# Performance work log

Measured on AMD Instinct MI355X. Metric: run time of the kernel, lower is better.

## Reference

```python
import jax, jax.numpy as jnp
import numpy as np

NUM_HEADS = 8

def setup_inputs() -> dict:
    key = jax.random.key(0)
    qkv = jax.random.normal(key, (8, 1536, 2048), dtype=jnp.float32)
    return {"qkv": qkv}

def reference(qkv) -> jnp.ndarray:
    bs, width, length = qkv.shape
    ch = width // (3 * NUM_HEADS)
    qkv_r = qkv.reshape(bs * NUM_HEADS, 3 * ch, length)
    q, k, v = jnp.split(qkv_r, 3, axis=1)  # each [bs*H, ch, length]
    scale = 1.0 / jnp.sqrt(jnp.sqrt(jnp.float32(ch)))
    # scores [bs*H, t, s]
    weight = jnp.einsum('bct,bcs->bts', q * scale, k * scale)
    weight = jax.nn.softmax(weight.astype(jnp.float32), axis=-1).astype(qkv.dtype)
    a = jnp.einsum('bts,bcs->bct', weight, v)  # [bs*H, ch, length]
    return a.reshape(bs, -1, length)
```

## Files before the change

### kernel.cpp

```cpp
#include <hip/hip_runtime.h>
#include <hip/hip_fp16.h>


typedef _Float16 half8 __attribute__((ext_vector_type(8)));
typedef _Float16 half4 __attribute__((ext_vector_type(4)));
typedef float floatx4 __attribute__((ext_vector_type(4)));

__global__ __launch_bounds__(256, 4) void attn_kernel(const float* __restrict__ qkv,
                                                      float* __restrict__ out)
{
    __shared__ _Float16 Kt[64 * 64];
    __shared__ _Float16 Vt[64 * 64];
    __shared__ _Float16 Pt[128 * 64];

    const int tid  = threadIdx.x;
    const int wave = tid >> 6;
    const int lane = tid & 63;
    const int llo  = lane & 15;
    const int lhi  = lane >> 4;

    const int blk  = blockIdx.x;
    const int slot = blk >> 3;
    const int bh   = (blk & 7) * 8 + (slot >> 4);
    const int tile = slot & 15;
    const int t0   = tile * 128;

    const float* qb = qkv + (size_t)bh * 393216;
    const float* kb = qb + 131072;
    const float* vb = qb + 262144;

    const float C  = 0.125f * 1.44269504088896f;
    const float B2 = 6.0f;

    half8 qf[2][2];
    const int twbase = t0 + wave * 32;
    #pragma unroll
    for (int nt = 0; nt < 2; ++nt) {
        const int t = twbase + nt * 16 + llo;
        #pragma unroll
        for (int ck = 0; ck < 2; ++ck)
            #pragma unroll
            for (int j = 0; j < 8; ++j) {
                const int c = ck * 32 + lhi * 8 + j;
                qf[nt][ck][j] = (_Float16)(qb[c * 2048 + t] * C);
            }
    }

    const int kc4 = (tid >> 4) * 4;
    const int ksq = (tid & 15) * 4;
    const int vc  = tid >> 4;
    const int vs  = (tid & 15) * 4;

    int kwoff[4];
    #pragma unroll
    for (int sr = 0; sr < 4; ++sr) {
        const int s  = ksq + sr;
        const int sw = ((s >> 2) ^ s) & 7;
        kwoff[sr] = s * 64 + ((((kc4 >> 3) ^ sw) & 7) << 3) + (kc4 & 7);
    }
    int vwoff[4];
    #pragma unroll
    for (int i = 0; i < 4; ++i) {
        const int c = vc + 16 * i;
        vwoff[i] = c * 64 + ((((vs >> 3) ^ (c & 7)) & 7) << 3) + (vs & 7);
    }
    int kroff[4][2];
    #pragma unroll
    for (int ms = 0; ms < 4; ++ms) {
        const int s  = ms * 16 + llo;
        const int sw = ((s >> 2) ^ s) & 7;
        kroff[ms][0] = s * 64 + (((lhi ^ sw) & 7) << 3);
        kroff[ms][1] = s * 64 + ((((lhi + 4) ^ sw) & 7) << 3);
    }
    int pwoff[2][4];
    #pragma unroll
    for (int nt = 0; nt < 2; ++nt) {
        const int row = wave * 32 + nt * 16 + llo;
        #pragma unroll
        for (int ms = 0; ms < 4; ++ms)
            pwoff[nt][ms] = row * 64 + ((((2 * ms + (lhi >> 1)) ^ (llo & 7)) & 7) << 3)
                          + 4 * (lhi & 1);
    }
    int proff[2][2];
    #pragma unroll
    for (int nt = 0; nt < 2; ++nt) {
        const int row = wave * 32 + nt * 16 + llo;
        #pragma unroll
        for (int sk = 0; sk < 2; ++sk)
            proff[nt][sk] = row * 64 + ((((sk * 4 + lhi) ^ (llo & 7)) & 7) << 3);
    }
    int vroff[4][2];
    #pragma unroll
    for (int mc = 0; mc < 4; ++mc) {
        const int row = mc * 16 + llo;
        #pragma unroll
        for (int sk = 0; sk < 2; ++sk)
            vroff[mc][sk] = row * 64 + ((((sk * 4 + lhi) ^ (llo & 7)) & 7) << 3);
    }

    floatx4 kr[4], vr[4];
    auto loadKV = [&](int s0) {
        #pragma unroll
        for (int r = 0; r < 4; ++r)
            kr[r] = *reinterpret_cast<const floatx4*>(kb + (kc4 + r) * 2048 + s0 + ksq);
        #pragma unroll
        for (int i = 0; i < 4; ++i)
            vr[i] = *reinterpret_cast<const floatx4*>(vb + (vc + 16 * i) * 2048 + s0 + vs);
    };
    auto storeKV = [&]() {
        #pragma unroll
        for (int sr = 0; sr < 4; ++sr) {
            half4 h = { (_Float16)kr[0][sr], (_Float16)kr[1][sr],
                        (_Float16)kr[2][sr], (_Float16)kr[3][sr] };
            *reinterpret_cast<half4*>(&Kt[kwoff[sr]]) = h;
        }
        #pragma unroll
        for (int i = 0; i < 4; ++i) {
            half4 h = { (_Float16)vr[i][0], (_Float16)vr[i][1],
                        (_Float16)vr[i][2], (_Float16)vr[i][3] };
            *reinterpret_cast<half4*>(&Vt[vwoff[i]]) = h;
        }
    };

    floatx4 O[2][4];
    #pragma unroll
    for (int nt = 0; nt < 2; ++nt)
        #pragma unroll
        for (int mc = 0; mc < 4; ++mc)
            O[nt][mc] = (floatx4){0.f, 0.f, 0.f, 0.f};
    float l_run[2] = {0.f, 0.f};

    loadKV(0);

    for (int it = 0; it < 32; ++it) {
        __syncthreads();
        storeKV();
        __syncthreads();
        if (it + 1 < 32) loadKV((it + 1) * 64);

        #pragma unroll
        for (int ms = 0; ms < 4; ++ms) {
            half8 a0 = *reinterpret_cast<const half8*>(&Kt[kroff[ms][0]]);
            half8 a1 = *reinterpret_cast<const half8*>(&Kt[kroff[ms][1]]);
            #pragma unroll
            for (int nt = 0; nt < 2; ++nt) {
                floatx4 acc = (floatx4){-B2, -B2, -B2, -B2};
                acc = __builtin_amdgcn_mfma_f32_16x16x32_f16(a0, qf[nt][0], acc, 0, 0, 0);
                acc = __builtin_amdgcn_mfma_f32_16x16x32_f16(a1, qf[nt][1], acc, 0, 0, 0);
                half4 ph;
                float l = 0.f;
                #pragma unroll
                for (int r = 0; r < 4; ++r) {
                    const float p = __builtin_amdgcn_exp2f(acc[r]);
                    l += p;
                    ph[r] = (_Float16)p;
                }
                l_run[nt] += l;
                *reinterpret_cast<half4*>(&Pt[pwoff[nt][ms]]) = ph;
            }
        }

        #pragma unroll
        for (int sk = 0; sk < 2; ++sk) {
            half8 bp[2];
            #pragma unroll
            for (int nt = 0; nt < 2; ++nt)
                bp[nt] = *reinterpret_cast<const half8*>(&Pt[proff[nt][sk]]);
            #pragma unroll
            for (int mc = 0; mc < 4; ++mc) {
                half8 av = *reinterpret_cast<const half8*>(&Vt[vroff[mc][sk]]);
                #pragma unroll
                for (int nt = 0; nt < 2; ++nt)
                    O[nt][mc] = __builtin_amdgcn_mfma_f32_16x16x32_f16(av, bp[nt], O[nt][mc], 0, 0, 0);
            }
        }
    }

    float* ob = out + (size_t)bh * 131072;
    #pragma unroll
    for (int nt = 0; nt < 2; ++nt) {
        float l = l_run[nt];
        l += __shfl_xor(l, 16, 64);
        l += __shfl_xor(l, 32, 64);
        const float inv = 1.0f / l;
        const int t = twbase + nt * 16 + llo;
        #pragma unroll
        for (int mc = 0; mc < 4; ++mc)
            #pragma unroll
            for (int r = 0; r < 4; ++r) {
                const int c = mc * 16 + lhi * 4 + r;
                ob[c * 2048 + t] = O[nt][mc][r] * inv;
            }
    }
}

extern "C" void kernel_launch(void* const* d_in, const int* in_sizes, int n_in,
                              void* d_out, int out_size, void* d_ws, size_t ws_size,
                              hipStream_t stream) {
    const float* qkv = (const float*)d_in[0];
    float* out = (float*)d_out;
    attn_kernel<<<dim3(1024), dim3(256), 0, stream>>>(qkv, out);
}
```

Before: 221.2 us.

## Keep softmax probabilities in registers and feed 16x16x16 MFMA directly

Removes the shared-memory round trip for the probability tile P. The exp outputs of the QK^T MFMA are packed to fp16 in registers and used directly as the B operand of 16x16x16 MFMAs for the PV product, with the V reads laid out to match. It also switches the fp32-to-fp16 conversions to packed round-toward-zero conversions. This drops LDS traffic and the Pt buffer, which lowers shared memory use. In exchange it issues twice as many smaller-K MFMAs and uses RTZ rounding instead of round-to-nearest.

```diff
diff --git a/kernel.cpp b/kernel.cpp
--- a/kernel.cpp
+++ b/kernel.cpp
@@ -4,6 +4,7 @@
 
 typedef _Float16 half8 __attribute__((ext_vector_type(8)));
 typedef _Float16 half4 __attribute__((ext_vector_type(4)));
+typedef _Float16 half2_t __attribute__((ext_vector_type(2)));
 typedef float floatx4 __attribute__((ext_vector_type(4)));
 
 __global__ __launch_bounds__(256, 4) void attn_kernel(const float* __restrict__ qkv,
@@ -11,7 +12,6 @@
 {
     __shared__ _Float16 Kt[64 * 64];
     __shared__ _Float16 Vt[64 * 64];
-    __shared__ _Float16 Pt[128 * 64];
 
     const int tid  = threadIdx.x;
     const int wave = tid >> 6;
@@ -72,30 +72,11 @@
         kroff[ms][0] = s * 64 + (((lhi ^ sw) & 7) << 3);
         kroff[ms][1] = s * 64 + ((((lhi + 4) ^ sw) & 7) << 3);
     }
-    int pwoff[2][4];
+    int vroff_in[4];
     #pragma unroll
-    for (int nt = 0; nt < 2; ++nt) {
-        const int row = wave * 32 + nt * 16 + llo;
-        #pragma unroll
-        for (int ms = 0; ms < 4; ++ms)
-            pwoff[nt][ms] = row * 64 + ((((2 * ms + (lhi >> 1)) ^ (llo & 7)) & 7) << 3)
-                          + 4 * (lhi & 1);
-    }
-    int proff[2][2];
-    #pragma unroll
-    for (int nt = 0; nt < 2; ++nt) {
-        const int row = wave * 32 + nt * 16 + llo;
-        #pragma unroll
-        for (int sk = 0; sk < 2; ++sk)
-            proff[nt][sk] = row * 64 + ((((sk * 4 + lhi) ^ (llo & 7)) & 7) << 3);
-    }
-    int vroff[4][2];
-    #pragma unroll
-    for (int mc = 0; mc < 4; ++mc) {
-        const int row = mc * 16 + llo;
-        #pragma unroll
-        for (int sk = 0; sk < 2; ++sk)
-            vroff[mc][sk] = row * 64 + ((((sk * 4 + lhi) ^ (llo & 7)) & 7) << 3);
+    for (int ms = 0; ms < 4; ++ms) {
+        const int pg = ((2 * ms + (lhi >> 1)) ^ (llo & 7)) & 7;
+        vroff_in[ms] = llo * 64 + (pg << 3) + ((lhi & 1) << 2);
     }
 
     floatx4 kr[4], vr[4];
@@ -110,14 +91,16 @@
     auto storeKV = [&]() {
         #pragma unroll
         for (int sr = 0; sr < 4; ++sr) {
-            half4 h = { (_Float16)kr[0][sr], (_Float16)kr[1][sr],
-                        (_Float16)kr[2][sr], (_Float16)kr[3][sr] };
+            half2_t lo = __builtin_bit_cast(half2_t, __builtin_amdgcn_cvt_pkrtz(kr[0][sr], kr[1][sr]));
+            half2_t hi = __builtin_bit_cast(half2_t, __builtin_amdgcn_cvt_pkrtz(kr[2][sr], kr[3][sr]));
+            half4 h = { lo[0], lo[1], hi[0], hi[1] };
             *reinterpret_cast<half4*>(&Kt[kwoff[sr]]) = h;
         }
         #pragma unroll
         for (int i = 0; i < 4; ++i) {
-            half4 h = { (_Float16)vr[i][0], (_Float16)vr[i][1],
-                        (_Float16)vr[i][2], (_Float16)vr[i][3] };
+            half2_t lo = __builtin_bit_cast(half2_t, __builtin_amdgcn_cvt_pkrtz(vr[i][0], vr[i][1]));
+            half2_t hi = __builtin_bit_cast(half2_t, __builtin_amdgcn_cvt_pkrtz(vr[i][2], vr[i][3]));
+            half4 h = { lo[0], lo[1], hi[0], hi[1] };
             *reinterpret_cast<half4*>(&Vt[vwoff[i]]) = h;
         }
     };
@@ -142,36 +125,26 @@
         for (int ms = 0; ms < 4; ++ms) {
             half8 a0 = *reinterpret_cast<const half8*>(&Kt[kroff[ms][0]]);
             half8 a1 = *reinterpret_cast<const half8*>(&Kt[kroff[ms][1]]);
+            half4 pf[2];
             #pragma unroll
             for (int nt = 0; nt < 2; ++nt) {
                 floatx4 acc = (floatx4){-B2, -B2, -B2, -B2};
                 acc = __builtin_amdgcn_mfma_f32_16x16x32_f16(a0, qf[nt][0], acc, 0, 0, 0);
                 acc = __builtin_amdgcn_mfma_f32_16x16x32_f16(a1, qf[nt][1], acc, 0, 0, 0);
-                half4 ph;
-                float l = 0.f;
-                #pragma unroll
-                for (int r = 0; r < 4; ++r) {
-                    const float p = __builtin_amdgcn_exp2f(acc[r]);
-                    l += p;
-                    ph[r] = (_Float16)p;
-                }
-                l_run[nt] += l;
-                *reinterpret_cast<half4*>(&Pt[pwoff[nt][ms]]) = ph;
+                const float p0 = __builtin_amdgcn_exp2f(acc[0]);
+                const float p1 = __builtin_amdgcn_exp2f(acc[1]);
+                const float p2 = __builtin_amdgcn_exp2f(acc[2]);
+                const float p3 = __builtin_amdgcn_exp2f(acc[3]);
+                l_run[nt] += (p0 + p1) + (p2 + p3);
+                half2_t lo = __builtin_bit_cast(half2_t, __builtin_amdgcn_cvt_pkrtz(p0, p1));
+                half2_t hi = __builtin_bit_cast(half2_t, __builtin_amdgcn_cvt_pkrtz(p2, p3));
+                pf[nt] = (half4){ lo[0], lo[1], hi[0], hi[1] };
             }
-        }
-
-        #pragma unroll
-        for (int sk = 0; sk < 2; ++sk) {
-            half8 bp[2];
-            #pragma unroll
-            for (int nt = 0; nt < 2; ++nt)
-                bp[nt] = *reinterpret_cast<const half8*>(&Pt[proff[nt][sk]]);
             #pragma unroll
             for (int mc = 0; mc < 4; ++mc) {
-                half8 av = *reinterpret_cast<const half8*>(&Vt[vroff[mc][sk]]);
-                #pragma unroll
-                for (int nt = 0; nt < 2; ++nt)
-                    O[nt][mc] = __builtin_amdgcn_mfma_f32_16x16x32_f16(av, bp[nt], O[nt][mc], 0, 0, 0);
+                half4 av = *reinterpret_cast<const half4*>(&Vt[mc * 1024 + vroff_in[ms]]);
+                O[0][mc] = __builtin_amdgcn_mfma_f32_16x16x16f16(av, pf[0], O[0][mc], 0, 0, 0);
+                O[1][mc] = __builtin_amdgcn_mfma_f32_16x16x16f16(av, pf[1], O[1][mc], 0, 0, 0);
             }
         }
     }
```

Result: slower. 239.0 us (+8.1%).

## Pre-convert K/V to swizzled fp16 and stream tiles via global_load_lds double buffer

Applied to the files above, without the earlier changes.

Adds a prep kernel that converts K and V to fp16 once, in the swizzled LDS tile layout, and stores them in the workspace. The attention kernel then DMAs those tiles directly into double-buffered LDS with global_load_lds, which drops the per-block fp32 loads, conversions and LDS stores along with one barrier per iteration. Softmax conversion now uses packed cvt_pkrtz. This costs an extra launch plus workspace traffic, and doubles the LDS used for K/V, which may reduce occupancy.

```diff
diff --git a/kernel.cpp b/kernel.cpp
--- a/kernel.cpp
+++ b/kernel.cpp
@@ -4,14 +4,68 @@
 
 typedef _Float16 half8 __attribute__((ext_vector_type(8)));
 typedef _Float16 half4 __attribute__((ext_vector_type(4)));
+typedef _Float16 half2_t __attribute__((ext_vector_type(2)));
 typedef float floatx4 __attribute__((ext_vector_type(4)));
 
+#define AS1 __attribute__((address_space(1)))
+#define AS3 __attribute__((address_space(3)))
+#define GLLDS(g, l) __builtin_amdgcn_global_load_lds((const AS1 void*)(g), (AS3 void*)(l), 16, 0, 0)
+
+__global__ __launch_bounds__(256) void prep_kernel(const float* __restrict__ qkv,
+                                                   _Float16* __restrict__ ws16)
+{
+    const int tid   = threadIdx.x;
+    const int blk   = blockIdx.x;
+    const int bh    = blk >> 5;
+    const int stile = blk & 31;
+    const int s0    = stile * 64;
+
+    const float* kb = qkv + (size_t)bh * 393216 + 131072;
+    const float* vb = qkv + (size_t)bh * 393216 + 262144;
+    _Float16* wk = ws16 + (size_t)bh * 262144 + stile * 4096;
+    _Float16* wv = wk + 131072;
+
+    const int kc4 = (tid >> 4) * 4;
+    const int ksq = (tid & 15) * 4;
+    const int vc  = tid >> 4;
+    const int vs  = (tid & 15) * 4;
+
+    floatx4 kr[4], vr[4];
+    #pragma unroll
+    for (int r = 0; r < 4; ++r)
+        kr[r] = *reinterpret_cast<const floatx4*>(kb + (kc4 + r) * 2048 + s0 + ksq);
+    #pragma unroll
+    for (int i = 0; i < 4; ++i)
+        vr[i] = *reinterpret_cast<const floatx4*>(vb + (vc + 16 * i) * 2048 + s0 + vs);
+
+    #pragma unroll
+    for (int sr = 0; sr < 4; ++sr) {
+        const int s  = ksq + sr;
+        const int sw = ((s >> 2) ^ s) & 7;
+        const int off = s * 64 + ((((kc4 >> 3) ^ sw) & 7) << 3) + (kc4 & 7);
+        half2_t lo = __builtin_bit_cast(half2_t, __builtin_amdgcn_cvt_pkrtz(kr[0][sr], kr[1][sr]));
+        half2_t hi = __builtin_bit_cast(half2_t, __builtin_amdgcn_cvt_pkrtz(kr[2][sr], kr[3][sr]));
+        half4 h = { lo[0], lo[1], hi[0], hi[1] };
+        *reinterpret_cast<half4*>(&wk[off]) = h;
+    }
+    #pragma unroll
+    for (int i = 0; i < 4; ++i) {
+        const int c = vc + 16 * i;
+        const int off = c * 64 + ((((vs >> 3) ^ (c & 7)) & 7) << 3) + (vs & 7);
+        half2_t lo = __builtin_bit_cast(half2_t, __builtin_amdgcn_cvt_pkrtz(vr[i][0], vr[i][1]));
+        half2_t hi = __builtin_bit_cast(half2_t, __builtin_amdgcn_cvt_pkrtz(vr[i][2], vr[i][3]));
+        half4 h = { lo[0], lo[1], hi[0], hi[1] };
+        *reinterpret_cast<half4*>(&wv[off]) = h;
+    }
+}
+
 __global__ __launch_bounds__(256, 4) void attn_kernel(const float* __restrict__ qkv,
+                                                      const _Float16* __restrict__ ws16,
                                                       float* __restrict__ out)
 {
-    __shared__ _Float16 Kt[64 * 64];
-    __shared__ _Float16 Vt[64 * 64];
-    __shared__ _Float16 Pt[128 * 64];
+    __shared__ _Float16 KtB[2][4096];
+    __shared__ _Float16 VtB[2][4096];
+    __shared__ _Float16 Pt[8192];
 
     const int tid  = threadIdx.x;
     const int wave = tid >> 6;
@@ -26,8 +80,8 @@
     const int t0   = tile * 128;
 
     const float* qb = qkv + (size_t)bh * 393216;
-    const float* kb = qb + 131072;
-    const float* vb = qb + 262144;
+    const _Float16* wkt = ws16 + (size_t)bh * 262144;
+    const _Float16* wvt = wkt + 131072;
 
     const float C  = 0.125f * 1.44269504088896f;
     const float B2 = 6.0f;
@@ -46,24 +100,6 @@
             }
     }
 
-    const int kc4 = (tid >> 4) * 4;
-    const int ksq = (tid & 15) * 4;
-    const int vc  = tid >> 4;
-    const int vs  = (tid & 15) * 4;
-
-    int kwoff[4];
-    #pragma unroll
-    for (int sr = 0; sr < 4; ++sr) {
-        const int s  = ksq + sr;
-        const int sw = ((s >> 2) ^ s) & 7;
-        kwoff[sr] = s * 64 + ((((kc4 >> 3) ^ sw) & 7) << 3) + (kc4 & 7);
-    }
-    int vwoff[4];
-    #pragma unroll
-    for (int i = 0; i < 4; ++i) {
-        const int c = vc + 16 * i;
-        vwoff[i] = c * 64 + ((((vs >> 3) ^ (c & 7)) & 7) << 3) + (vs & 7);
-    }
     int kroff[4][2];
     #pragma unroll
     for (int ms = 0; ms < 4; ++ms) {
@@ -98,28 +134,15 @@
             vroff[mc][sk] = row * 64 + ((((sk * 4 + lhi) ^ (llo & 7)) & 7) << 3);
     }
 
-    floatx4 kr[4], vr[4];
-    auto loadKV = [&](int s0) {
-        #pragma unroll
-        for (int r = 0; r < 4; ++r)
-            kr[r] = *reinterpret_cast<const floatx4*>(kb + (kc4 + r) * 2048 + s0 + ksq);
-        #pragma unroll
-        for (int i = 0; i < 4; ++i)
-            vr[i] = *reinterpret_cast<const floatx4*>(vb + (vc + 16 * i) * 2048 + s0 + vs);
-    };
-    auto storeKV = [&]() {
-        #pragma unroll
-        for (int sr = 0; sr < 4; ++sr) {
-            half4 h = { (_Float16)kr[0][sr], (_Float16)kr[1][sr],
-                        (_Float16)kr[2][sr], (_Float16)kr[3][sr] };
-            *reinterpret_cast<half4*>(&Kt[kwoff[sr]]) = h;
-        }
-        #pragma unroll
-        for (int i = 0; i < 4; ++i) {
-            half4 h = { (_Float16)vr[i][0], (_Float16)vr[i][1],
-                        (_Float16)vr[i][2], (_Float16)vr[i][3] };
-            *reinterpret_cast<half4*>(&Vt[vwoff[i]]) = h;
-        }
+    auto dma = [&](int it, int b) {
+        const char* gk = (const char*)(wkt + it * 4096) + wave * 2048 + lane * 16;
+        const char* gv = (const char*)(wvt + it * 4096) + wave * 2048 + lane * 16;
+        char* lk = (char*)(&KtB[b][0]) + wave * 2048;
+        char* lv = (char*)(&VtB[b][0]) + wave * 2048;
+        GLLDS(gk,        lk);
+        GLLDS(gk + 1024, lk + 1024);
+        GLLDS(gv,        lv);
+        GLLDS(gv + 1024, lv + 1024);
     };
 
     floatx4 O[2][4];
@@ -130,13 +153,14 @@
             O[nt][mc] = (floatx4){0.f, 0.f, 0.f, 0.f};
     float l_run[2] = {0.f, 0.f};
 
-    loadKV(0);
+    dma(0, 0);
+    __syncthreads();
 
     for (int it = 0; it < 32; ++it) {
-        __syncthreads();
-        storeKV();
-        __syncthreads();
-        if (it + 1 < 32) loadKV((it + 1) * 64);
+        if (it + 1 < 32) dma(it + 1, (it + 1) & 1);
+
+        const _Float16* Kt = KtB[it & 1];
+        const _Float16* Vt = VtB[it & 1];
 
         #pragma unroll
         for (int ms = 0; ms < 4; ++ms) {
@@ -147,15 +171,14 @@
                 floatx4 acc = (floatx4){-B2, -B2, -B2, -B2};
                 acc = __builtin_amdgcn_mfma_f32_16x16x32_f16(a0, qf[nt][0], acc, 0, 0, 0);
                 acc = __builtin_amdgcn_mfma_f32_16x16x32_f16(a1, qf[nt][1], acc, 0, 0, 0);
-                half4 ph;
-                float l = 0.f;
-                #pragma unroll
-                for (int r = 0; r < 4; ++r) {
-                    const float p = __builtin_amdgcn_exp2f(acc[r]);
-                    l += p;
-                    ph[r] = (_Float16)p;
-                }
-                l_run[nt] += l;
+                const float p0 = __builtin_amdgcn_exp2f(acc[0]);
+                const float p1 = __builtin_amdgcn_exp2f(acc[1]);
+                const float p2 = __builtin_amdgcn_exp2f(acc[2]);
+                const float p3 = __builtin_amdgcn_exp2f(acc[3]);
+                l_run[nt] += (p0 + p1) + (p2 + p3);
+                half2_t lo = __builtin_bit_cast(half2_t, __builtin_amdgcn_cvt_pkrtz(p0, p1));
+                half2_t hi = __builtin_bit_cast(half2_t, __builtin_amdgcn_cvt_pkrtz(p2, p3));
+                half4 ph = { lo[0], lo[1], hi[0], hi[1] };
                 *reinterpret_cast<half4*>(&Pt[pwoff[nt][ms]]) = ph;
             }
         }
@@ -174,6 +197,8 @@
                     O[nt][mc] = __builtin_amdgcn_mfma_f32_16x16x32_f16(av, bp[nt], O[nt][mc], 0, 0, 0);
             }
         }
+
+        __syncthreads();
     }
 
     float* ob = out + (size_t)bh * 131072;
@@ -199,5 +224,7 @@
                               hipStream_t stream) {
     const float* qkv = (const float*)d_in[0];
     float* out = (float*)d_out;
-    attn_kernel<<<dim3(1024), dim3(256), 0, stream>>>(qkv, out);
+    _Float16* ws16 = (_Float16*)d_ws;
+    prep_kernel<<<dim3(2048), dim3(256), 0, stream>>>(qkv, ws16);
+    attn_kernel<<<dim3(1024), dim3(256), 0, stream>>>(qkv, ws16, out);
 }
```

After: 252.6 us. 14.2% more time.
